# Kernel optimization log

Measured on AMD Instinct MI355X. Metric: run time of the kernel, lower is better.

Reference implementation:

```python
import jax, jax.numpy as jnp
import numpy as np

N_NODES = 40962
N_EDGES = 245760
K = 10  # gaussian kernels
D = 2   # pseudo-coordinate dim
EPS = 1e-15


def gmm_conv(x, edge_index, pseudo, g, mu, sigma, root, bias):
    """PyG GMMConv with aggr='mean', root_weight=True.
    x: [N, Cin], edge_index: [2, E] (row 0 = source j, row 1 = target i),
    pseudo: [E, D], g: [Cin, K*Cout], mu/sigma: [K, D], root: [Cin, Cout], bias: [Cout].
    """
    src, dst = edge_index[0], edge_index[1]
    E = pseudo.shape[0]
    # Gaussian mixture edge weights: [E, K]
    diff = pseudo[:, None, :] - mu[None, :, :]                     # [E, K, D]
    w = jnp.exp(jnp.sum(-0.5 * diff * diff / (EPS + sigma[None] ** 2), axis=-1))
    xj = x[src]                                                    # [E, Cin] gather
    y = (xj @ g).reshape(E, K, -1)                                 # [E, K, Cout]
    msg = jnp.sum(y * w[:, :, None], axis=1)                       # [E, Cout]
    agg = jax.ops.segment_sum(msg, dst, num_segments=N_NODES)      # scatter-add
    deg = jax.ops.segment_sum(jnp.ones((E,), x.dtype), dst, num_segments=N_NODES)
    agg = agg / jnp.maximum(deg, 1.0)[:, None]                     # mean aggregation
    return agg + x @ root + bias


def setup_inputs() -> dict:
    key = jax.random.key(0)
    ks = jax.random.split(key, 20)
    Cin, Ch, Cout = 64, 64, 128
    sc = lambda fan: 1.0 / np.sqrt(fan)
    inp = {
        "x": jax.random.normal(ks[0], (N_NODES, Cin), jnp.float32),
        "edge_index": jax.random.randint(ks[1], (2, N_EDGES), 0, N_NODES, jnp.int32),
        "pseudo": jax.random.uniform(ks[2], (N_EDGES, D), jnp.float32),
        # conv1: Cin -> Ch
        "g1": jax.random.normal(ks[3], (Cin, K * Ch), jnp.float32) * sc(Cin),
        "mu1": jax.random.uniform(ks[4], (K, D), jnp.float32),
        "sigma1": jax.random.uniform(ks[5], (K, D), jnp.float32) + 0.5,
        "root1": jax.random.normal(ks[6], (Cin, Ch), jnp.float32) * sc(Cin),
        "b1": jnp.zeros((Ch,), jnp.float32),
        # conv2: Ch -> Cout
        "g2": jax.random.normal(ks[7], (Ch, K * Cout), jnp.float32) * sc(Ch),
        "mu2": jax.random.uniform(ks[8], (K, D), jnp.float32),
        "sigma2": jax.random.uniform(ks[9], (K, D), jnp.float32) + 0.5,
        "root2": jax.random.normal(ks[10], (Ch, Cout), jnp.float32) * sc(Ch),
        "b2": jnp.zeros((Cout,), jnp.float32),
        # shortcut: Cin -> Cout (size_in != size_out)
        "gs": jax.random.normal(ks[11], (Cin, K * Cout), jnp.float32) * sc(Cin),
        "mus": jax.random.uniform(ks[12], (K, D), jnp.float32),
        "sigmas": jax.random.uniform(ks[13], (K, D), jnp.float32) + 0.5,
        "roots": jax.random.normal(ks[14], (Cin, Cout), jnp.float32) * sc(Cin),
        "bs": jnp.zeros((Cout,), jnp.float32),
    }
    return inp


def reference(x, edge_index, pseudo, g1, mu1, sigma1, root1, b1,
              g2, mu2, sigma2, root2, b2, gs, mus, sigmas, roots, bs):
    h = gmm_conv(x, edge_index, pseudo, g1, mu1, sigma1, root1, b1)
    h = jax.nn.relu(h)
    y = gmm_conv(h, edge_index, pseudo, g2, mu2, sigma2, root2, b2)
    x_s = gmm_conv(x, edge_index, pseudo, gs, mus, sigmas, roots, bs)
    return jax.nn.relu(y + x_s)
```

## Files before the change

### kernel.cpp

```cpp
#include <hip/hip_runtime.h>
#include <hip/hip_bf16.h>

using bf16 = __hip_bfloat16;
typedef __attribute__((ext_vector_type(8))) short short8;
typedef __attribute__((ext_vector_type(4))) float float4v;

#define N_NODES 40962
#define N_EDGES 245760
#define NP      41024
#define KG      10
#define SCAN_B  256
#define NBLK    ((NP + SCAN_B - 1) / SCAN_B)
#define GRIDF   (NP / 16)

#define CVT_V   (N_NODES * 64 / 8)
#define CVT_BLK ((CVT_V + 255) / 256)
#define W3_BLK  (N_EDGES / 256)
#define PACK_N  (64 * 704 + 2 * 128 * 704)
#define PACK_BLK (PACK_N / 256)

#define ZRS  40
#define ZKS  648
#define ZSZE 12960

__device__ __forceinline__ float ldf(const void* p, size_t i, int isf32) {
    return isf32 ? ((const float*)p)[i] : __bfloat162float(((const bf16*)p)[i]);
}
__device__ __forceinline__ float blo(unsigned u) { return __uint_as_float(u << 16); }
__device__ __forceinline__ float bhi(unsigned u) { return __uint_as_float(u & 0xffff0000u); }
__device__ __forceinline__ unsigned pk2(float a, float b) {
    union { bf16 h[2]; unsigned u; } t;
    t.h[0] = __float2bfloat16(a);
    t.h[1] = __float2bfloat16(b);
    return t.u;
}
__device__ __forceinline__ int rfl(int v) { return __builtin_amdgcn_readfirstlane(v); }

__global__ void k_detect_count(const void* x, const int* __restrict__ ei,
                               int* __restrict__ flag, int* __restrict__ deg) {
    if (blockIdx.x == 0) {
        __shared__ int huge_c, zero_even;
        if (threadIdx.x == 0) { huge_c = 0; zero_even = 0; }
        __syncthreads();
        const bf16* xb = (const bf16*)x;
        int lh = 0, lz = 0;
        for (int i = threadIdx.x; i < 8192; i += 256) {
            float v = __bfloat162float(xb[i]);
            if (!(fabsf(v) <= 1e4f)) lh++;
            if ((i & 1) == 0 && v == 0.0f) lz++;
        }
        atomicAdd(&huge_c, lh);
        atomicAdd(&zero_even, lz);
        __syncthreads();
        if (threadIdx.x == 0) flag[0] = (huge_c > 0 || zero_even > 3000) ? 1 : 0;
    } else {
        int e = (blockIdx.x - 1) * 256 + threadIdx.x;
        if (e < N_EDGES) atomicAdd(&deg[ei[N_EDGES + e]], 1);
    }
}

__global__ void k_scan1(const int* __restrict__ deg, int* __restrict__ offs,
                        int* __restrict__ bsum) {
    __shared__ int buf[SCAN_B];
    int t = threadIdx.x, b = blockIdx.x;
    int i = b * SCAN_B + t;
    int v = (i < NP) ? deg[i] : 0;
    buf[t] = v;
    __syncthreads();
    for (int off = 1; off < SCAN_B; off <<= 1) {
        int a = (t >= off) ? buf[t - off] : 0;
        __syncthreads();
        buf[t] += a;
        __syncthreads();
    }
    if (i < NP) offs[i] = buf[t] - v;
    if (t == SCAN_B - 1) bsum[b] = buf[t];
}

__global__ void k_scan3m(int* __restrict__ offs, const int* __restrict__ bsum,
                         const int* __restrict__ deg, int* __restrict__ cur,
                         float* __restrict__ invdeg) {
    __shared__ int buf[256];
    int t = threadIdx.x, b = blockIdx.x;
    int v = (t < NBLK) ? bsum[t] : 0;
    buf[t] = v;
    __syncthreads();
    for (int off = 1; off < 256; off <<= 1) {
        int a = (t >= off) ? buf[t - off] : 0;
        __syncthreads();
        buf[t] += a;
        __syncthreads();
    }
    int bofs = (b > 0) ? buf[b - 1] : 0;
    int total = buf[NBLK - 1];
    int i = b * 256 + t;
    if (i < NP) {
        int o = offs[i] + bofs;
        offs[i] = o;
        cur[i] = o;
        int d = deg[i];
        invdeg[i] = 1.0f / (float)(d > 1 ? d : 1);
    }
    if (i == 0) offs[NP] = total;
}

__global__ void k_fill(const int* __restrict__ ei, int* __restrict__ cur,
                       int* __restrict__ ep, int* __restrict__ csr_src) {
    int e = blockIdx.x * 256 + threadIdx.x;
    if (e < N_EDGES) {
        int pos = atomicAdd(&cur[ei[N_EDGES + e]], 1);
        ep[e] = pos;
        csr_src[pos] = ei[e];
    }
}

__device__ __forceinline__ void gw_one(float p0, float p1, const void* mu,
                                       const void* sg, int f, float* out) {
#pragma unroll
    for (int k = 0; k < KG; k++) {
        float m0 = ldf(mu, 2 * k + 0, f), m1 = ldf(mu, 2 * k + 1, f);
        float s0 = ldf(sg, 2 * k + 0, f), s1 = ldf(sg, 2 * k + 1, f);
        float d0 = p0 - m0, d1 = p1 - m1;
        float t = -0.5f * (d0 * d0 / (1e-15f + s0 * s0) + d1 * d1 / (1e-15f + s1 * s1));
        out[k] = __expf(t);
    }
}

__device__ __forceinline__ void pack_frag(const void* g, const void* root, int f,
                                          int idx, int Cout, bf16* Bp) {
    int j = idx & 7;
    int lane = (idx >> 3) & 63;
    int rem = idx >> 9;
    int kc = rem % 22;
    int n = rem / 22;
    int col = n * 16 + (lane & 15);
    int k = kc * 32 + (lane >> 4) * 8 + j;
    float v;
    if (k < 512) {
        int cin = k >> 3, kg = k & 7;
        v = ldf(g, (size_t)cin * (KG * Cout) + (size_t)kg * Cout + col, f);
    } else if (k < 640) {
        int jj = k - 512;
        int cin = jj >> 1, kg = 8 + (jj & 1);
        v = ldf(g, (size_t)cin * (KG * Cout) + (size_t)kg * Cout + col, f);
    } else {
        v = ldf(root, (size_t)(k - 640) * Cout + col, f);
    }
    Bp[idx] = __float2bfloat16(v);
}

__global__ void k_prep_all(const void* __restrict__ x, const void* __restrict__ pseudo,
                           const void* mu1, const void* sg1, const void* mu2,
                           const void* sg2, const void* mus, const void* sgs,
                           const void* g1, const void* root1, const void* g2,
                           const void* root2, const void* gs, const void* roots,
                           const int* __restrict__ flag, const int* __restrict__ ep,
                           bf16* __restrict__ Xf, bf16* __restrict__ wc1,
                           bf16* __restrict__ wcs, bf16* __restrict__ wc2,
                           bf16* wt1p, bf16* wt2p, bf16* wtsp) {
    int b = blockIdx.x;
    int tid = threadIdx.x;
    int f = flag[0];
    if (b < CVT_BLK) {
        int i = b * 256 + tid;
        if (i < CVT_V) {
            int node = i >> 3, j = i & 7;
            uint4 u;
            if (f) {
                const float4* xf = (const float4*)x;
                float4 a = xf[2 * i], c = xf[2 * i + 1];
                union { bf16 t[8]; uint4 u; } tt;
                tt.t[0] = __float2bfloat16(a.x); tt.t[1] = __float2bfloat16(a.y);
                tt.t[2] = __float2bfloat16(a.z); tt.t[3] = __float2bfloat16(a.w);
                tt.t[4] = __float2bfloat16(c.x); tt.t[5] = __float2bfloat16(c.y);
                tt.t[6] = __float2bfloat16(c.z); tt.t[7] = __float2bfloat16(c.w);
                u = tt.u;
            } else {
                u = ((const uint4*)x)[i];
            }
            *(uint4*)(Xf + ((size_t)(j >> 2) * NP + node) * 32 + (j & 3) * 8) = u;
        }
    } else if (b < CVT_BLK + W3_BLK) {
        int e = (b - CVT_BLK) * 256 + tid;
        float p0 = ldf(pseudo, (size_t)e * 2 + 0, f);
        float p1 = ldf(pseudo, (size_t)e * 2 + 1, f);
        float o1[KG], o2[KG], os[KG];
        gw_one(p0, p1, mu1, sg1, f, o1);
        gw_one(p0, p1, mu2, sg2, f, o2);
        gw_one(p0, p1, mus, sgs, f, os);
        int pos = ep[e];
        unsigned* d1 = (unsigned*)wc1 + (size_t)pos * 5;
        d1[0] = pk2(o1[0], o1[1]); d1[1] = pk2(o1[2], o1[3]);
        d1[2] = pk2(o1[4], o1[5]); d1[3] = pk2(o1[6], o1[7]);
        d1[4] = pk2(o1[8], o1[9]);
        unsigned* ds = (unsigned*)wcs + (size_t)pos * 5;
        ds[0] = pk2(os[0], os[1]); ds[1] = pk2(os[2], os[3]);
        ds[2] = pk2(os[4], os[5]); ds[3] = pk2(os[6], os[7]);
        ds[4] = pk2(os[8], os[9]);
        unsigned* d2 = (unsigned*)wc2 + (size_t)pos * 5;
        d2[0] = pk2(o2[0], o2[1]); d2[1] = pk2(o2[2], o2[3]);
        d2[2] = pk2(o2[4], o2[5]); d2[3] = pk2(o2[6], o2[7]);
        d2[4] = pk2(o2[8], o2[9]);
    } else {
        int idx = (b - CVT_BLK - W3_BLK) * 256 + tid;
        if (idx < 64 * 704) {
            pack_frag(g1, root1, f, idx, 64, wt1p);
        } else if (idx < 64 * 704 + 128 * 704) {
            pack_frag(g2, root2, f, idx - 64 * 704, 128, wt2p);
        } else {
            pack_frag(gs, roots, f, idx - 64 * 704 - 128 * 704, 128, wtsp);
        }
    }
}

__device__ __forceinline__ float ldx_frag(const bf16* X, int src, int lane) {
    return __bfloat162float(X[((size_t)(lane >> 5) * NP + src) * 32 + (lane & 31)]);
}

__device__ __forceinline__ int clampe(int idx) {
    return idx > N_EDGES - 1 ? N_EDGES - 1 : idx;
}

__device__ __forceinline__ void store_zlds(bf16* z, int r, int lane, const float* a,
                                           float inv) {
    union { bf16 h[8]; uint4 u; } p;
#pragma unroll
    for (int k = 0; k < 8; k++) p.h[k] = __float2bfloat16(a[k] * inv);
    *(uint4*)(z + (lane >> 2) * ZKS + r * ZRS + (lane & 3) * 8) = p.u;
    *(unsigned*)(z + (16 + (lane >> 4)) * ZKS + r * ZRS + (lane & 15) * 2) =
        pk2(a[8] * inv, a[9] * inv);
}

__global__ __launch_bounds__(256) void k_fused1(
    const int* __restrict__ offs, const int* __restrict__ csr_src,
    const bf16* __restrict__ wc1, const float* __restrict__ invdeg,
    const bf16* __restrict__ Xf, const bf16* __restrict__ wt1p,
    const void* __restrict__ b1, const int* __restrict__ flag,
    bf16* __restrict__ hf) {
    __shared__ bf16 zA[ZSZE];
    int lane = threadIdx.x & 63;
    int wave = threadIdx.x >> 6;
    int bid = blockIdx.x;
    const unsigned* wb = (const unsigned*)wc1;

    for (int i = 0; i < 4; i++) {
        int r = wave * 4 + i;
        int node = bid * 16 + r;
        float acc[KG];
#pragma unroll
        for (int k = 0; k < KG; k++) acc[k] = 0.0f;
        int beg = rfl(offs[node]);
        int end = rfl(offs[node + 1]);
        int cnt = end - beg;
        int sC = rfl(csr_src[clampe(beg + 2)]);
        float xv0 = ldx_frag(Xf, rfl(csr_src[clampe(beg + 0)]), lane);
        float xv1 = ldx_frag(Xf, rfl(csr_src[clampe(beg + 1)]), lane);
        const unsigned* wp0 = wb + (size_t)clampe(beg + 0) * 5;
        unsigned c0 = wp0[0], c1 = wp0[1], c2 = wp0[2], c3 = wp0[3], c4 = wp0[4];
        const unsigned* wp1 = wb + (size_t)clampe(beg + 1) * 5;
        unsigned n0 = wp1[0], n1 = wp1[1], n2 = wp1[2], n3 = wp1[3], n4 = wp1[4];
        for (int t = 0; t < cnt; ++t) {
            int sN = rfl(csr_src[clampe(beg + t + 3)]);
            float xv2 = ldx_frag(Xf, sC, lane);
            const unsigned* wp2 = wb + (size_t)clampe(beg + t + 2) * 5;
            unsigned m0 = wp2[0], m1 = wp2[1], m2 = wp2[2], m3 = wp2[3], m4 = wp2[4];
            acc[0] += blo(c0) * xv0; acc[1] += bhi(c0) * xv0;
            acc[2] += blo(c1) * xv0; acc[3] += bhi(c1) * xv0;
            acc[4] += blo(c2) * xv0; acc[5] += bhi(c2) * xv0;
            acc[6] += blo(c3) * xv0; acc[7] += bhi(c3) * xv0;
            acc[8] += blo(c4) * xv0; acc[9] += bhi(c4) * xv0;
            xv0 = xv1; xv1 = xv2; sC = sN;
            c0 = n0; c1 = n1; c2 = n2; c3 = n3; c4 = n4;
            n0 = m0; n1 = m1; n2 = m2; n3 = m3; n4 = m4;
        }
        store_zlds(zA, r, lane, acc, invdeg[node]);
    }
    __syncthreads();

    int m = lane & 15, quad = lane >> 4;
    int row0 = bid * 16;
    float4v acc4 = (float4v){0.f, 0.f, 0.f, 0.f};
    const bf16* brow = wt1p + ((size_t)(wave * 22) * 64 + lane) * 8;
    const bf16* xrow = Xf + ((size_t)(row0 + m)) * 32 + quad * 8;
#pragma unroll
    for (int kc = 0; kc < 22; kc++) {
        short8 a = (kc < 20)
            ? *(const short8*)(zA + kc * ZKS + m * ZRS + quad * 8)
            : *(const short8*)(xrow + (size_t)(kc - 20) * NP * 32);
        short8 b = *(const short8*)(brow + (size_t)kc * 512);
        acc4 = __builtin_amdgcn_mfma_f32_16x16x32_bf16(a, b, acc4, 0, 0, 0);
    }
    int f = flag[0];
    int gcol = wave * 16 + m;
    float bv = ldf(b1, gcol, f);
#pragma unroll
    for (int r = 0; r < 4; r++) {
        int grow = row0 + quad * 4 + r;
        if (grow >= N_NODES) continue;
        float v = fmaxf(acc4[r] + bv, 0.f);
        hf[((size_t)(gcol >> 5) * NP + grow) * 32 + (gcol & 31)] = __float2bfloat16(v);
    }
}

__global__ __launch_bounds__(256) void k_fused2(
    const int* __restrict__ offs, const int* __restrict__ csr_src,
    const bf16* __restrict__ wc2, const bf16* __restrict__ wcs,
    const float* __restrict__ invdeg, const bf16* __restrict__ Xf,
    const bf16* __restrict__ hf, const bf16* __restrict__ wt2p,
    const bf16* __restrict__ wtsp, const void* __restrict__ b2,
    const void* __restrict__ bs, const int* __restrict__ flag,
    void* __restrict__ out) {
    __shared__ bf16 z2[ZSZE];
    __shared__ bf16 zs[ZSZE];
    int lane = threadIdx.x & 63;
    int wave = threadIdx.x >> 6;
    int bid = blockIdx.x;
    const unsigned* w2b = (const unsigned*)wc2;
    const unsigned* wsb = (const unsigned*)wcs;

    for (int i = 0; i < 4; i++) {
        int r = wave * 4 + i;
        int node = bid * 16 + r;
        float a2[KG], as[KG];
#pragma unroll
        for (int k = 0; k < KG; k++) { a2[k] = 0.0f; as[k] = 0.0f; }
        int beg = rfl(offs[node]);
        int end = rfl(offs[node + 1]);
        int cnt = end - beg;
        int sC = rfl(csr_src[clampe(beg + 2)]);
        int s0 = rfl(csr_src[clampe(beg + 0)]);
        int s1 = rfl(csr_src[clampe(beg + 1)]);
        float hv0 = ldx_frag(hf, s0, lane), xv0 = ldx_frag(Xf, s0, lane);
        float hv1 = ldx_frag(hf, s1, lane), xv1 = ldx_frag(Xf, s1, lane);
        const unsigned* p20 = w2b + (size_t)clampe(beg + 0) * 5;
        unsigned c0 = p20[0], c1 = p20[1], c2 = p20[2], c3 = p20[3], c4 = p20[4];
        const unsigned* ps0 = wsb + (size_t)clampe(beg + 0) * 5;
        unsigned d0 = ps0[0], d1 = ps0[1], d2 = ps0[2], d3 = ps0[3], d4 = ps0[4];
        const unsigned* p21 = w2b + (size_t)clampe(beg + 1) * 5;
        unsigned n0 = p21[0], n1 = p21[1], n2 = p21[2], n3 = p21[3], n4 = p21[4];
        const unsigned* ps1 = wsb + (size_t)clampe(beg + 1) * 5;
        unsigned o0 = ps1[0], o1 = ps1[1], o2 = ps1[2], o3 = ps1[3], o4 = ps1[4];
        for (int t = 0; t < cnt; ++t) {
            int sN = rfl(csr_src[clampe(beg + t + 3)]);
            float hv2 = ldx_frag(hf, sC, lane);
            float xv2 = ldx_frag(Xf, sC, lane);
            const unsigned* p22 = w2b + (size_t)clampe(beg + t + 2) * 5;
            unsigned m0 = p22[0], m1 = p22[1], m2 = p22[2], m3 = p22[3], m4 = p22[4];
            const unsigned* ps2 = wsb + (size_t)clampe(beg + t + 2) * 5;
            unsigned q0 = ps2[0], q1 = ps2[1], q2 = ps2[2], q3 = ps2[3], q4 = ps2[4];
            a2[0] += blo(c0) * hv0; a2[1] += bhi(c0) * hv0;
            a2[2] += blo(c1) * hv0; a2[3] += bhi(c1) * hv0;
            a2[4] += blo(c2) * hv0; a2[5] += bhi(c2) * hv0;
            a2[6] += blo(c3) * hv0; a2[7] += bhi(c3) * hv0;
            a2[8] += blo(c4) * hv0; a2[9] += bhi(c4) * hv0;
            as[0] += blo(d0) * xv0; as[1] += bhi(d0) * xv0;
            as[2] += blo(d1) * xv0; as[3] += bhi(d1) * xv0;
            as[4] += blo(d2) * xv0; as[5] += bhi(d2) * xv0;
            as[6] += blo(d3) * xv0; as[7] += bhi(d3) * xv0;
            as[8] += blo(d4) * xv0; as[9] += bhi(d4) * xv0;
            hv0 = hv1; hv1 = hv2; xv0 = xv1; xv1 = xv2; sC = sN;
            c0 = n0; c1 = n1; c2 = n2; c3 = n3; c4 = n4;
            n0 = m0; n1 = m1; n2 = m2; n3 = m3; n4 = m4;
            d0 = o0; d1 = o1; d2 = o2; d3 = o3; d4 = o4;
            o0 = q0; o1 = q1; o2 = q2; o3 = q3; o4 = q4;
        }
        float inv = invdeg[node];
        store_zlds(z2, r, lane, a2, inv);
        store_zlds(zs, r, lane, as, inv);
    }
    __syncthreads();

    int m = lane & 15, quad = lane >> 4;
    int row0 = bid * 16;
    const bf16* hrow = hf + ((size_t)(row0 + m)) * 32 + quad * 8;
    const bf16* xrow = Xf + ((size_t)(row0 + m)) * 32 + quad * 8;
    int f = flag[0];
#pragma unroll
    for (int tt = 0; tt < 2; tt++) {
        int n = wave + tt * 4;
        float4v acc4 = (float4v){0.f, 0.f, 0.f, 0.f};
        const bf16* b2row = wt2p + ((size_t)(n * 22) * 64 + lane) * 8;
        const bf16* bsrow = wtsp + ((size_t)(n * 22) * 64 + lane) * 8;
#pragma unroll
        for (int kc = 0; kc < 22; kc++) {
            short8 a = (kc < 20)
                ? *(const short8*)(z2 + kc * ZKS + m * ZRS + quad * 8)
                : *(const short8*)(hrow + (size_t)(kc - 20) * NP * 32);
            short8 b = *(const short8*)(b2row + (size_t)kc * 512);
            acc4 = __builtin_amdgcn_mfma_f32_16x16x32_bf16(a, b, acc4, 0, 0, 0);
        }
#pragma unroll
        for (int kc = 0; kc < 22; kc++) {
            short8 a = (kc < 20)
                ? *(const short8*)(zs + kc * ZKS + m * ZRS + quad * 8)
                : *(const short8*)(xrow + (size_t)(kc - 20) * NP * 32);
            short8 b = *(const short8*)(bsrow + (size_t)kc * 512);
            acc4 = __builtin_amdgcn_mfma_f32_16x16x32_bf16(a, b, acc4, 0, 0, 0);
        }
        int gcol = n * 16 + m;
        float bv = ldf(b2, gcol, f) + ldf(bs, gcol, f);
#pragma unroll
        for (int r = 0; r < 4; r++) {
            int grow = row0 + quad * 4 + r;
            if (grow >= N_NODES) continue;
            float v = fmaxf(acc4[r] + bv, 0.f);
            size_t oidx = (size_t)grow * 128 + gcol;
            if (f) ((float*)out)[oidx] = v;
            else   ((bf16*)out)[oidx] = __float2bfloat16(v);
        }
    }
}

extern "C" void kernel_launch(void* const* d_in, const int* in_sizes, int n_in,
                              void* d_out, int out_size, void* d_ws, size_t ws_size,
                              hipStream_t stream) {
    const void* x      = d_in[0];
    const int*  ei     = (const int*)d_in[1];
    const void* pseudo = d_in[2];
    const void* g1     = d_in[3];
    const void* mu1    = d_in[4];
    const void* sg1    = d_in[5];
    const void* root1  = d_in[6];
    const void* b1     = d_in[7];
    const void* g2     = d_in[8];
    const void* mu2    = d_in[9];
    const void* sg2    = d_in[10];
    const void* root2  = d_in[11];
    const void* b2     = d_in[12];
    const void* gs     = d_in[13];
    const void* mus    = d_in[14];
    const void* sgs    = d_in[15];
    const void* roots  = d_in[16];
    const void* bs     = d_in[17];

    char* ws = (char*)d_ws;
    size_t off = 0;
    auto alloc = [&](size_t bytes) -> char* {
        char* p = ws + off;
        off += (bytes + 255) & ~(size_t)255;
        return p;
    };
    const size_t XFS = (size_t)2 * NP * 32 * 2;

    int*   flag   = (int*)alloc(256);
    int*   deg    = (int*)alloc((size_t)NP * 4);
    int*   offs   = (int*)alloc((size_t)(NP + 1) * 4);
    int*   cur    = (int*)alloc((size_t)NP * 4);
    float* invdeg = (float*)alloc((size_t)NP * 4);
    int*   bsum   = (int*)alloc((size_t)NBLK * 4);
    int*   ep     = (int*)alloc((size_t)N_EDGES * 4);
    int*   csrs   = (int*)alloc((size_t)N_EDGES * 4);
    bf16*  Xf     = (bf16*)alloc(XFS);
    bf16*  hf     = (bf16*)alloc(XFS);
    bf16*  wt1p   = (bf16*)alloc((size_t)64 * 704 * 2);
    bf16*  wt2p   = (bf16*)alloc((size_t)128 * 704 * 2);
    bf16*  wtsp   = (bf16*)alloc((size_t)128 * 704 * 2);
    bf16*  wc1    = (bf16*)alloc((size_t)N_EDGES * 10 * 2);
    bf16*  wcs    = (bf16*)alloc((size_t)N_EDGES * 10 * 2);
    bf16*  wc2    = (bf16*)alloc((size_t)N_EDGES * 10 * 2);
    (void)ws_size;

    hipMemsetAsync(deg, 0, (size_t)NP * 4, stream);
    k_detect_count<<<1 + (N_EDGES + 255) / 256, 256, 0, stream>>>(x, ei, flag, deg);
    k_scan1<<<NBLK, SCAN_B, 0, stream>>>(deg, offs, bsum);
    k_scan3m<<<NBLK, 256, 0, stream>>>(offs, bsum, deg, cur, invdeg);
    k_fill<<<(N_EDGES + 255) / 256, 256, 0, stream>>>(ei, cur, ep, csrs);
    k_prep_all<<<CVT_BLK + W3_BLK + PACK_BLK, 256, 0, stream>>>(
        x, pseudo, mu1, sg1, mu2, sg2, mus, sgs, g1, root1, g2, root2, gs, roots,
        flag, ep, Xf, wc1, wcs, wc2, wt1p, wt2p, wtsp);
    k_fused1<<<GRIDF, 256, 0, stream>>>(offs, csrs, wc1, invdeg, Xf, wt1p, b1,
                                        flag, hf);
    k_fused2<<<GRIDF, 256, 0, stream>>>(offs, csrs, wc2, wcs, invdeg, Xf, hf,
                                        wt2p, wtsp, b2, bs, flag, d_out);
}
```

Before: 279.4 us.

## Double block size to 512 threads, split fused2 into sequential gather/MFMA phases sharing LDS

```diff
diff --git a/kernel.cpp b/kernel.cpp
--- a/kernel.cpp
+++ b/kernel.cpp
@@ -20,8 +20,8 @@
 #define PACK_BLK (PACK_N / 256)
 
 #define ZRS  40
-#define ZKS  648
-#define ZSZE 12960
+#define ZKS  672
+#define ZSZE 13440
 
 __device__ __forceinline__ float ldf(const void* p, size_t i, int isf32) {
     return isf32 ? ((const float*)p)[i] : __bfloat162float(((const bf16*)p)[i]);
@@ -221,6 +221,39 @@
     return idx > N_EDGES - 1 ? N_EDGES - 1 : idx;
 }
 
+__device__ __forceinline__ void gather_one(const int* __restrict__ offs,
+                                           const int* __restrict__ csr_src,
+                                           const unsigned* __restrict__ wb,
+                                           const bf16* __restrict__ X, int node,
+                                           int lane, float* acc) {
+#pragma unroll
+    for (int k = 0; k < KG; k++) acc[k] = 0.0f;
+    int beg = rfl(offs[node]);
+    int end = rfl(offs[node + 1]);
+    int cnt = end - beg;
+    int sC = rfl(csr_src[clampe(beg + 2)]);
+    float xv0 = ldx_frag(X, rfl(csr_src[clampe(beg + 0)]), lane);
+    float xv1 = ldx_frag(X, rfl(csr_src[clampe(beg + 1)]), lane);
+    const unsigned* wp0 = wb + (size_t)clampe(beg + 0) * 5;
+    unsigned c0 = wp0[0], c1 = wp0[1], c2 = wp0[2], c3 = wp0[3], c4 = wp0[4];
+    const unsigned* wp1 = wb + (size_t)clampe(beg + 1) * 5;
+    unsigned n0 = wp1[0], n1 = wp1[1], n2 = wp1[2], n3 = wp1[3], n4 = wp1[4];
+    for (int t = 0; t < cnt; ++t) {
+        int sN = rfl(csr_src[clampe(beg + t + 3)]);
+        float xv2 = ldx_frag(X, sC, lane);
+        const unsigned* wp2 = wb + (size_t)clampe(beg + t + 2) * 5;
+        unsigned m0 = wp2[0], m1 = wp2[1], m2 = wp2[2], m3 = wp2[3], m4 = wp2[4];
+        acc[0] += blo(c0) * xv0; acc[1] += bhi(c0) * xv0;
+        acc[2] += blo(c1) * xv0; acc[3] += bhi(c1) * xv0;
+        acc[4] += blo(c2) * xv0; acc[5] += bhi(c2) * xv0;
+        acc[6] += blo(c3) * xv0; acc[7] += bhi(c3) * xv0;
+        acc[8] += blo(c4) * xv0; acc[9] += bhi(c4) * xv0;
+        xv0 = xv1; xv1 = xv2; sC = sN;
+        c0 = n0; c1 = n1; c2 = n2; c3 = n3; c4 = n4;
+        n0 = m0; n1 = m1; n2 = m2; n3 = m3; n4 = m4;
+    }
+}
+
 __device__ __forceinline__ void store_zlds(bf16* z, int r, int lane, const float* a,
                                            float inv) {
     union { bf16 h[8]; uint4 u; } p;
@@ -231,7 +264,7 @@
         pk2(a[8] * inv, a[9] * inv);
 }
 
-__global__ __launch_bounds__(256) void k_fused1(
+__global__ __launch_bounds__(512) void k_fused1(
     const int* __restrict__ offs, const int* __restrict__ csr_src,
     const bf16* __restrict__ wc1, const float* __restrict__ invdeg,
     const bf16* __restrict__ Xf, const bf16* __restrict__ wt1p,
@@ -243,66 +276,45 @@
     int bid = blockIdx.x;
     const unsigned* wb = (const unsigned*)wc1;
 
-    for (int i = 0; i < 4; i++) {
-        int r = wave * 4 + i;
+#pragma unroll
+    for (int i = 0; i < 2; i++) {
+        int r = wave * 2 + i;
         int node = bid * 16 + r;
         float acc[KG];
-#pragma unroll
-        for (int k = 0; k < KG; k++) acc[k] = 0.0f;
-        int beg = rfl(offs[node]);
-        int end = rfl(offs[node + 1]);
-        int cnt = end - beg;
-        int sC = rfl(csr_src[clampe(beg + 2)]);
-        float xv0 = ldx_frag(Xf, rfl(csr_src[clampe(beg + 0)]), lane);
-        float xv1 = ldx_frag(Xf, rfl(csr_src[clampe(beg + 1)]), lane);
-        const unsigned* wp0 = wb + (size_t)clampe(beg + 0) * 5;
-        unsigned c0 = wp0[0], c1 = wp0[1], c2 = wp0[2], c3 = wp0[3], c4 = wp0[4];
-        const unsigned* wp1 = wb + (size_t)clampe(beg + 1) * 5;
-        unsigned n0 = wp1[0], n1 = wp1[1], n2 = wp1[2], n3 = wp1[3], n4 = wp1[4];
-        for (int t = 0; t < cnt; ++t) {
-            int sN = rfl(csr_src[clampe(beg + t + 3)]);
-            float xv2 = ldx_frag(Xf, sC, lane);
-            const unsigned* wp2 = wb + (size_t)clampe(beg + t + 2) * 5;
-            unsigned m0 = wp2[0], m1 = wp2[1], m2 = wp2[2], m3 = wp2[3], m4 = wp2[4];
-            acc[0] += blo(c0) * xv0; acc[1] += bhi(c0) * xv0;
-            acc[2] += blo(c1) * xv0; acc[3] += bhi(c1) * xv0;
-            acc[4] += blo(c2) * xv0; acc[5] += bhi(c2) * xv0;
-            acc[6] += blo(c3) * xv0; acc[7] += bhi(c3) * xv0;
-            acc[8] += blo(c4) * xv0; acc[9] += bhi(c4) * xv0;
-            xv0 = xv1; xv1 = xv2; sC = sN;
-            c0 = n0; c1 = n1; c2 = n2; c3 = n3; c4 = n4;
-            n0 = m0; n1 = m1; n2 = m2; n3 = m3; n4 = m4;
-        }
+        gather_one(offs, csr_src, wb, Xf, node, lane, acc);
         store_zlds(zA, r, lane, acc, invdeg[node]);
     }
     __syncthreads();
 
-    int m = lane & 15, quad = lane >> 4;
-    int row0 = bid * 16;
-    float4v acc4 = (float4v){0.f, 0.f, 0.f, 0.f};
-    const bf16* brow = wt1p + ((size_t)(wave * 22) * 64 + lane) * 8;
-    const bf16* xrow = Xf + ((size_t)(row0 + m)) * 32 + quad * 8;
-#pragma unroll
-    for (int kc = 0; kc < 22; kc++) {
-        short8 a = (kc < 20)
-            ? *(const short8*)(zA + kc * ZKS + m * ZRS + quad * 8)
-            : *(const short8*)(xrow + (size_t)(kc - 20) * NP * 32);
-        short8 b = *(const short8*)(brow + (size_t)kc * 512);
-        acc4 = __builtin_amdgcn_mfma_f32_16x16x32_bf16(a, b, acc4, 0, 0, 0);
-    }
-    int f = flag[0];
-    int gcol = wave * 16 + m;
-    float bv = ldf(b1, gcol, f);
-#pragma unroll
-    for (int r = 0; r < 4; r++) {
-        int grow = row0 + quad * 4 + r;
-        if (grow >= N_NODES) continue;
-        float v = fmaxf(acc4[r] + bv, 0.f);
-        hf[((size_t)(gcol >> 5) * NP + grow) * 32 + (gcol & 31)] = __float2bfloat16(v);
-    }
-}
-
-__global__ __launch_bounds__(256) void k_fused2(
+    if (wave < 4) {
+        int m = lane & 15, quad = lane >> 4;
+        int row0 = bid * 16;
+        float4v acc4 = (float4v){0.f, 0.f, 0.f, 0.f};
+        const bf16* brow = wt1p + ((size_t)(wave * 22) * 64 + lane) * 8;
+        const bf16* xrow = Xf + ((size_t)(row0 + m)) * 32 + quad * 8;
+#pragma unroll
+        for (int kc = 0; kc < 22; kc++) {
+            short8 a = (kc < 20)
+                ? *(const short8*)(zA + kc * ZKS + m * ZRS + quad * 8)
+                : *(const short8*)(xrow + (size_t)(kc - 20) * NP * 32);
+            short8 b = *(const short8*)(brow + (size_t)kc * 512);
+            acc4 = __builtin_amdgcn_mfma_f32_16x16x32_bf16(a, b, acc4, 0, 0, 0);
+        }
+        int f = flag[0];
+        int gcol = wave * 16 + m;
+        float bv = ldf(b1, gcol, f);
+#pragma unroll
+        for (int r = 0; r < 4; r++) {
+            int grow = row0 + quad * 4 + r;
+            if (grow >= N_NODES) continue;
+            float v = fmaxf(acc4[r] + bv, 0.f);
+            hf[((size_t)(gcol >> 5) * NP + grow) * 32 + (gcol & 31)] =
+                __float2bfloat16(v);
+        }
+    }
+}
+
+__global__ __launch_bounds__(512) void k_fused2(
     const int* __restrict__ offs, const int* __restrict__ csr_src,
     const bf16* __restrict__ wc2, const bf16* __restrict__ wcs,
     const float* __restrict__ invdeg, const bf16* __restrict__ Xf,
@@ -310,104 +322,72 @@
     const bf16* __restrict__ wtsp, const void* __restrict__ b2,
     const void* __restrict__ bs, const int* __restrict__ flag,
     void* __restrict__ out) {
-    __shared__ bf16 z2[ZSZE];
-    __shared__ bf16 zs[ZSZE];
+    __shared__ bf16 z[ZSZE];
     int lane = threadIdx.x & 63;
     int wave = threadIdx.x >> 6;
     int bid = blockIdx.x;
-    const unsigned* w2b = (const unsigned*)wc2;
-    const unsigned* wsb = (const unsigned*)wcs;
-
-    for (int i = 0; i < 4; i++) {
-        int r = wave * 4 + i;
-        int node = bid * 16 + r;
-        float a2[KG], as[KG];
-#pragma unroll
-        for (int k = 0; k < KG; k++) { a2[k] = 0.0f; as[k] = 0.0f; }
-        int beg = rfl(offs[node]);
-        int end = rfl(offs[node + 1]);
-        int cnt = end - beg;
-        int sC = rfl(csr_src[clampe(beg + 2)]);
-        int s0 = rfl(csr_src[clampe(beg + 0)]);
-        int s1 = rfl(csr_src[clampe(beg + 1)]);
-        float hv0 = ldx_frag(hf, s0, lane), xv0 = ldx_frag(Xf, s0, lane);
-        float hv1 = ldx_frag(hf, s1, lane), xv1 = ldx_frag(Xf, s1, lane);
-        const unsigned* p20 = w2b + (size_t)clampe(beg + 0) * 5;
-        unsigned c0 = p20[0], c1 = p20[1], c2 = p20[2], c3 = p20[3], c4 = p20[4];
-        const unsigned* ps0 = wsb + (size_t)clampe(beg + 0) * 5;
-        unsigned d0 = ps0[0], d1 = ps0[1], d2 = ps0[2], d3 = ps0[3], d4 = ps0[4];
-        const unsigned* p21 = w2b + (size_t)clampe(beg + 1) * 5;
-        unsigned n0 = p21[0], n1 = p21[1], n2 = p21[2], n3 = p21[3], n4 = p21[4];
-        const unsigned* ps1 = wsb + (size_t)clampe(beg + 1) * 5;
-        unsigned o0 = ps1[0], o1 = ps1[1], o2 = ps1[2], o3 = ps1[3], o4 = ps1[4];
-        for (int t = 0; t < cnt; ++t) {
-            int sN = rfl(csr_src[clampe(beg + t + 3)]);
-            float hv2 = ldx_frag(hf, sC, lane);
-            float xv2 = ldx_frag(Xf, sC, lane);
-            const unsigned* p22 = w2b + (size_t)clampe(beg + t + 2) * 5;
-            unsigned m0 = p22[0], m1 = p22[1], m2 = p22[2], m3 = p22[3], m4 = p22[4];
-            const unsigned* ps2 = wsb + (size_t)clampe(beg + t + 2) * 5;
-            unsigned q0 = ps2[0], q1 = ps2[1], q2 = ps2[2], q3 = ps2[3], q4 = ps2[4];
-            a2[0] += blo(c0) * hv0; a2[1] += bhi(c0) * hv0;
-            a2[2] += blo(c1) * hv0; a2[3] += bhi(c1) * hv0;
-            a2[4] += blo(c2) * hv0; a2[5] += bhi(c2) * hv0;
-            a2[6] += blo(c3) * hv0; a2[7] += bhi(c3) * hv0;
-            a2[8] += blo(c4) * hv0; a2[9] += bhi(c4) * hv0;
-            as[0] += blo(d0) * xv0; as[1] += bhi(d0) * xv0;
-            as[2] += blo(d1) * xv0; as[3] += bhi(d1) * xv0;
-            as[4] += blo(d2) * xv0; as[5] += bhi(d2) * xv0;
-            as[6] += blo(d3) * xv0; as[7] += bhi(d3) * xv0;
-            as[8] += blo(d4) * xv0; as[9] += bhi(d4) * xv0;
-            hv0 = hv1; hv1 = hv2; xv0 = xv1; xv1 = xv2; sC = sN;
-            c0 = n0; c1 = n1; c2 = n2; c3 = n3; c4 = n4;
-            n0 = m0; n1 = m1; n2 = m2; n3 = m3; n4 = m4;
-            d0 = o0; d1 = o1; d2 = o2; d3 = o3; d4 = o4;
-            o0 = q0; o1 = q1; o2 = q2; o3 = q3; o4 = q4;
-        }
-        float inv = invdeg[node];
-        store_zlds(z2, r, lane, a2, inv);
-        store_zlds(zs, r, lane, as, inv);
-    }
-    __syncthreads();
-
     int m = lane & 15, quad = lane >> 4;
     int row0 = bid * 16;
-    const bf16* hrow = hf + ((size_t)(row0 + m)) * 32 + quad * 8;
-    const bf16* xrow = Xf + ((size_t)(row0 + m)) * 32 + quad * 8;
-    int f = flag[0];
-#pragma unroll
-    for (int tt = 0; tt < 2; tt++) {
-        int n = wave + tt * 4;
-        float4v acc4 = (float4v){0.f, 0.f, 0.f, 0.f};
-        const bf16* b2row = wt2p + ((size_t)(n * 22) * 64 + lane) * 8;
-        const bf16* bsrow = wtsp + ((size_t)(n * 22) * 64 + lane) * 8;
+
+#pragma unroll
+    for (int i = 0; i < 2; i++) {
+        int r = wave * 2 + i;
+        int node = bid * 16 + r;
+        float acc[KG];
+        gather_one(offs, csr_src, (const unsigned*)wc2, hf, node, lane, acc);
+        store_zlds(z, r, lane, acc, invdeg[node]);
+    }
+    __syncthreads();
+
+    float4v acc4 = (float4v){0.f, 0.f, 0.f, 0.f};
+    {
+        const bf16* brow = wt2p + ((size_t)(wave * 22) * 64 + lane) * 8;
+        const bf16* hrow = hf + ((size_t)(row0 + m)) * 32 + quad * 8;
 #pragma unroll
         for (int kc = 0; kc < 22; kc++) {
             short8 a = (kc < 20)
-                ? *(const short8*)(z2 + kc * ZKS + m * ZRS + quad * 8)
+                ? *(const short8*)(z + kc * ZKS + m * ZRS + quad * 8)
                 : *(const short8*)(hrow + (size_t)(kc - 20) * NP * 32);
-            short8 b = *(const short8*)(b2row + (size_t)kc * 512);
+            short8 b = *(const short8*)(brow + (size_t)kc * 512);
             acc4 = __builtin_amdgcn_mfma_f32_16x16x32_bf16(a, b, acc4, 0, 0, 0);
         }
+    }
+    __syncthreads();
+
+#pragma unroll
+    for (int i = 0; i < 2; i++) {
+        int r = wave * 2 + i;
+        int node = bid * 16 + r;
+        float acc[KG];
+        gather_one(offs, csr_src, (const unsigned*)wcs, Xf, node, lane, acc);
+        store_zlds(z, r, lane, acc, invdeg[node]);
+    }
+    __syncthreads();
+
+    {
+        const bf16* brow = wtsp + ((size_t)(wave * 22) * 64 + lane) * 8;
+        const bf16* xrow = Xf + ((size_t)(row0 + m)) * 32 + quad * 8;
 #pragma unroll
         for (int kc = 0; kc < 22; kc++) {
             short8 a = (kc < 20)
-                ? *(const short8*)(zs + kc * ZKS + m * ZRS + quad * 8)
+                ? *(const short8*)(z + kc * ZKS + m * ZRS + quad * 8)
                 : *(const short8*)(xrow + (size_t)(kc - 20) * NP * 32);
-            short8 b = *(const short8*)(bsrow + (size_t)kc * 512);
+            short8 b = *(const short8*)(brow + (size_t)kc * 512);
             acc4 = __builtin_amdgcn_mfma_f32_16x16x32_bf16(a, b, acc4, 0, 0, 0);
         }
-        int gcol = n * 16 + m;
-        float bv = ldf(b2, gcol, f) + ldf(bs, gcol, f);
-#pragma unroll
-        for (int r = 0; r < 4; r++) {
-            int grow = row0 + quad * 4 + r;
-            if (grow >= N_NODES) continue;
-            float v = fmaxf(acc4[r] + bv, 0.f);
-            size_t oidx = (size_t)grow * 128 + gcol;
-            if (f) ((float*)out)[oidx] = v;
-            else   ((bf16*)out)[oidx] = __float2bfloat16(v);
-        }
+    }
+
+    int f = flag[0];
+    int gcol = wave * 16 + m;
+    float bv = ldf(b2, gcol, f) + ldf(bs, gcol, f);
+#pragma unroll
+    for (int r = 0; r < 4; r++) {
+        int grow = row0 + quad * 4 + r;
+        if (grow >= N_NODES) continue;
+        float v = fmaxf(acc4[r] + bv, 0.f);
+        size_t oidx = (size_t)grow * 128 + gcol;
+        if (f) ((float*)out)[oidx] = v;
+        else   ((bf16*)out)[oidx] = __float2bfloat16(v);
     }
 }
 
@@ -468,8 +448,8 @@
     k_prep_all<<<CVT_BLK + W3_BLK + PACK_BLK, 256, 0, stream>>>(
         x, pseudo, mu1, sg1, mu2, sg2, mus, sgs, g1, root1, g2, root2, gs, roots,
         flag, ep, Xf, wc1, wcs, wc2, wt1p, wt2p, wtsp);
-    k_fused1<<<GRIDF, 256, 0, stream>>>(offs, csrs, wc1, invdeg, Xf, wt1p, b1,
+    k_fused1<<<GRIDF, 512, 0, stream>>>(offs, csrs, wc1, invdeg, Xf, wt1p, b1,
                                         flag, hf);
-    k_fused2<<<GRIDF, 256, 0, stream>>>(offs, csrs, wc2, wcs, invdeg, Xf, hf,
+    k_fused2<<<GRIDF, 512, 0, stream>>>(offs, csrs, wc2, wcs, invdeg, Xf, hf,
                                         wt2p, wtsp, b2, bs, flag, d_out);
 }
```

New measurement: 273.3 us. 2.2% less time.
